# Kernel tuning notes

Measured on AMD Instinct MI355X. Metric: run time of the kernel, lower is better.

The kernel has to match this reference:

```python
import jax, jax.numpy as jnp
import numpy as np

N_BITS = 6
N_ENTRIES = 1 << N_BITS  # 64 LUT entries per node
B, IN, OUT = 1024, 1024, 2048


def setup_inputs() -> dict:
    key = jax.random.key(0)
    k1, k2, k3 = jax.random.split(key, 3)
    x = jax.random.uniform(k1, (B, IN), dtype=jnp.float32)          # soft bits in [0,1]
    lut_table = jax.random.normal(k2, (OUT, N_ENTRIES), dtype=jnp.float32)  # per-node LUT weights
    mapping = jax.random.randint(k3, (OUT, N_BITS), 0, IN, dtype=jnp.int32)  # wires per node
    return {"x": x, "lut_table": lut_table, "mapping": mapping}


def _lut_forward(x, lut_table, mapping):
    # get_mapping: gather n input wires per output node -> [B, OUT, n]
    mapped = x[:, mapping]
    # bits[k, j] = j-th bit of entry k  -> [2^n, n]
    bits = ((jnp.arange(N_ENTRIES)[:, None] >> jnp.arange(N_BITS)[None, :]) & 1
            ).astype(x.dtype)
    # Soft-AND probability of each LUT entry, built multiplicatively over the
    # n (=6) fan-in bits to avoid a [B,OUT,2^n,n] intermediate.
    probs = jnp.ones((x.shape[0], mapping.shape[0], N_ENTRIES), dtype=x.dtype)
    for j in range(N_BITS):
        xj = mapped[:, :, j][:, :, None]              # [B, OUT, 1]
        bj = bits[:, j][None, None, :]                # [1, 1, 2^n]
        probs = probs * (bj * xj + (1.0 - bj) * (1.0 - xj))
    # Expected LUT output per node: contract entry axis with learned table.
    return jnp.einsum('bok,ok->bo', probs, lut_table)


def reference(x, lut_table, mapping):
    return _lut_forward(x, lut_table, mapping)
```

## Files before the change

### kernel.cpp

```cpp
#include <hip/hip_runtime.h>

#define B_DIM   1024
#define IN_DIM  1024
#define OUT_DIM 2048
#define NBITS   6
#define NENT    64

__global__ __launch_bounds__(256) void transpose_x(const float* __restrict__ x,
                                                   float* __restrict__ xT) {
    __shared__ float tile[32][33];
    const int bx = blockIdx.x * 32;
    const int by = blockIdx.y * 32;
    const int tx = threadIdx.x & 31;
    const int ty = threadIdx.x >> 5;
#pragma unroll
    for (int i = 0; i < 4; i++) {
        const int r = by + ty + i * 8;
        tile[ty + i * 8][tx] = x[r * IN_DIM + bx + tx];
    }
    __syncthreads();
#pragma unroll
    for (int i = 0; i < 4; i++) {
        const int r = bx + ty + i * 8;
        xT[r * B_DIM + by + tx] = tile[tx][ty + i * 8];
    }
}

__global__ __launch_bounds__(256) void lut_fwd(const float* __restrict__ xsrc,
                                               const float* __restrict__ lut,
                                               const int* __restrict__ mapping,
                                               float* __restrict__ out,
                                               int sm, int sb) {
    __shared__ float slut[NENT];
    __shared__ int   smap[NBITS];
    const int o = blockIdx.y;
    const int b = blockIdx.x * 256 + threadIdx.x;

    if (threadIdx.x < NENT)  slut[threadIdx.x] = lut[o * NENT + threadIdx.x];
    if (threadIdx.x < NBITS) smap[threadIdx.x] = mapping[o * NBITS + threadIdx.x];
    __syncthreads();

    float xv[NBITS];
#pragma unroll
    for (int j = 0; j < NBITS; j++) {
        xv[j] = xsrc[smap[j] * sm + b * sb];
    }

    float v[NENT];
#pragma unroll
    for (int k = 0; k < NENT; k++) v[k] = slut[k];

#pragma unroll
    for (int j = 0; j < NBITS; j++) {
        const float xj = xv[j];
        const float om = 1.0f - xj;
#pragma unroll
        for (int m = 0; m < (NENT >> (j + 1)); m++) {
            v[m] = fmaf(v[2 * m + 1], xj, v[2 * m] * om);
        }
    }

    out[(size_t)b * OUT_DIM + o] = v[0];
}

extern "C" void kernel_launch(void* const* d_in, const int* in_sizes, int n_in,
                              void* d_out, int out_size, void* d_ws, size_t ws_size,
                              hipStream_t stream) {
    const float* x       = (const float*)d_in[0];
    const float* lut     = (const float*)d_in[1];
    const int*   mapping = (const int*)d_in[2];
    float*       out     = (float*)d_out;

    const size_t xt_bytes = (size_t)B_DIM * IN_DIM * sizeof(float);
    const dim3 grid(B_DIM / 256, OUT_DIM);

    if (ws_size >= xt_bytes) {
        float* xT = (float*)d_ws;
        const dim3 tgrid(IN_DIM / 32, B_DIM / 32);
        transpose_x<<<tgrid, 256, 0, stream>>>(x, xT);
        lut_fwd<<<grid, 256, 0, stream>>>(xT, lut, mapping, out, B_DIM, 1);
    } else {
        lut_fwd<<<grid, 256, 0, stream>>>(x, lut, mapping, out, 1, IN_DIM);
    }
}
```

Before: 77.13 us.

## Tile batch-by-output per block and coalesce output stores via shared memory

Replaces the one-output-per-block kernel with a 64x32 batch-by-output tile, where each wave handles 8 output nodes and stages its results in shared memory. The tile is then written back so consecutive threads store consecutive output columns, replacing the strided scattered stores. LUT and mapping reads use wave-uniform addresses, so they can be served as scalar loads instead of going through shared memory and a barrier. This raises register pressure and serializes 8 nodes per thread.

```diff
diff --git a/kernel.cpp b/kernel.cpp
--- a/kernel.cpp
+++ b/kernel.cpp
@@ -5,6 +5,10 @@
 #define OUT_DIM 2048
 #define NBITS   6
 #define NENT    64
+
+#define BT      64
+#define OT      32
+#define OPT     8
 
 __global__ __launch_bounds__(256) void transpose_x(const float* __restrict__ x,
                                                    float* __restrict__ xT) {
@@ -14,52 +18,88 @@
     const int tx = threadIdx.x & 31;
     const int ty = threadIdx.x >> 5;
 #pragma unroll
-    for (int i = 0; i < 4; i++) {
-        const int r = by + ty + i * 8;
-        tile[ty + i * 8][tx] = x[r * IN_DIM + bx + tx];
+    for (int i = 0; i < 4; i++)
+        tile[ty + i * 8][tx] = x[(by + ty + i * 8) * IN_DIM + bx + tx];
+    __syncthreads();
+#pragma unroll
+    for (int i = 0; i < 4; i++)
+        xT[(bx + ty + i * 8) * B_DIM + by + tx] = tile[tx][ty + i * 8];
+}
+
+__global__ __launch_bounds__(256, 4) void lut_fwd_t(const float* __restrict__ xT,
+                                                    const float* __restrict__ lut,
+                                                    const int* __restrict__ mapping,
+                                                    float* __restrict__ out) {
+    __shared__ float tile[BT][OT + 1];
+    const int tid = threadIdx.x;
+    const int tb  = tid & (BT - 1);
+    const int tg  = __builtin_amdgcn_readfirstlane(tid >> 6);
+    const int b0  = blockIdx.x * BT;
+    const int o0  = blockIdx.y * OT;
+    const int b   = b0 + tb;
+
+#pragma unroll
+    for (int i = 0; i < OPT; i++) {
+        const int o = o0 + tg * OPT + i;
+        const float* __restrict__ lr = lut + (size_t)o * NENT;
+        const int*   __restrict__ mp = mapping + (size_t)o * NBITS;
+
+        float xv[NBITS];
+#pragma unroll
+        for (int j = 0; j < NBITS; j++)
+            xv[j] = xT[(size_t)mp[j] * B_DIM + b];
+
+        float w[NENT / 2];
+        {
+            const float xj = xv[0], om = 1.0f - xj;
+#pragma unroll
+            for (int m = 0; m < NENT / 2; m++)
+                w[m] = fmaf(lr[2 * m + 1], xj, lr[2 * m] * om);
+        }
+#pragma unroll
+        for (int j = 1; j < NBITS; j++) {
+            const float xj = xv[j], om = 1.0f - xj;
+#pragma unroll
+            for (int m = 0; m < (NENT >> (j + 1)); m++)
+                w[m] = fmaf(w[2 * m + 1], xj, w[2 * m] * om);
+        }
+        tile[tb][tg * OPT + i] = w[0];
     }
     __syncthreads();
+
 #pragma unroll
-    for (int i = 0; i < 4; i++) {
-        const int r = bx + ty + i * 8;
-        xT[r * B_DIM + by + tx] = tile[tx][ty + i * 8];
+    for (int s = 0; s < (BT * OT) / 256; s++) {
+        const int f  = s * 256 + tid;
+        const int bb = f >> 5;
+        const int cc = f & (OT - 1);
+        out[(size_t)(b0 + bb) * OUT_DIM + o0 + cc] = tile[bb][cc];
     }
 }
 
-__global__ __launch_bounds__(256) void lut_fwd(const float* __restrict__ xsrc,
-                                               const float* __restrict__ lut,
-                                               const int* __restrict__ mapping,
-                                               float* __restrict__ out,
-                                               int sm, int sb) {
+__global__ __launch_bounds__(256) void lut_fwd_fallback(const float* __restrict__ x,
+                                                        const float* __restrict__ lut,
+                                                        const int* __restrict__ mapping,
+                                                        float* __restrict__ out) {
     __shared__ float slut[NENT];
     __shared__ int   smap[NBITS];
     const int o = blockIdx.y;
     const int b = blockIdx.x * 256 + threadIdx.x;
-
     if (threadIdx.x < NENT)  slut[threadIdx.x] = lut[o * NENT + threadIdx.x];
     if (threadIdx.x < NBITS) smap[threadIdx.x] = mapping[o * NBITS + threadIdx.x];
     __syncthreads();
-
     float xv[NBITS];
 #pragma unroll
-    for (int j = 0; j < NBITS; j++) {
-        xv[j] = xsrc[smap[j] * sm + b * sb];
-    }
-
+    for (int j = 0; j < NBITS; j++) xv[j] = x[(size_t)b * IN_DIM + smap[j]];
     float v[NENT];
 #pragma unroll
     for (int k = 0; k < NENT; k++) v[k] = slut[k];
-
 #pragma unroll
     for (int j = 0; j < NBITS; j++) {
-        const float xj = xv[j];
-        const float om = 1.0f - xj;
+        const float xj = xv[j], om = 1.0f - xj;
 #pragma unroll
-        for (int m = 0; m < (NENT >> (j + 1)); m++) {
+        for (int m = 0; m < (NENT >> (j + 1)); m++)
             v[m] = fmaf(v[2 * m + 1], xj, v[2 * m] * om);
-        }
     }
-
     out[(size_t)b * OUT_DIM + o] = v[0];
 }
 
@@ -72,14 +112,15 @@
     float*       out     = (float*)d_out;
 
     const size_t xt_bytes = (size_t)B_DIM * IN_DIM * sizeof(float);
-    const dim3 grid(B_DIM / 256, OUT_DIM);
 
     if (ws_size >= xt_bytes) {
         float* xT = (float*)d_ws;
         const dim3 tgrid(IN_DIM / 32, B_DIM / 32);
         transpose_x<<<tgrid, 256, 0, stream>>>(x, xT);
-        lut_fwd<<<grid, 256, 0, stream>>>(xT, lut, mapping, out, B_DIM, 1);
+        const dim3 grid(B_DIM / BT, OUT_DIM / OT);
+        lut_fwd_t<<<grid, 256, 0, stream>>>(xT, lut, mapping, out);
     } else {
-        lut_fwd<<<grid, 256, 0, stream>>>(x, lut, mapping, out, 1, IN_DIM);
+        const dim3 grid(B_DIM / 256, OUT_DIM);
+        lut_fwd_fallback<<<grid, 256, 0, stream>>>(x, lut, mapping, out);
     }
 }
```

Result: no change. 76.98 us (-0.2%).

## Fuse transpose into LUT kernel with Möbius-transformed tables and smem-staged x rows

Applied to the files above, without the earlier changes.

Drops the separate transpose kernel. Each thread now owns one output node and keeps that node's 64-entry table in registers, after converting it once with a Möbius (inclusion-exclusion) transform so each sample needs only a chain of fmas with no (1-x) terms. A block stages 16 rows of x in shared memory and gathers each node's six inputs from there, so output writes are coalesced along the node axis. The cost is heavy register use (64 coefficients plus 32 temporaries) and a 64KB+ shared tile that limits occupancy. The transformed-coefficient form may also differ slightly from the reference in rounding.

```diff
diff --git a/kernel.cpp b/kernel.cpp
--- a/kernel.cpp
+++ b/kernel.cpp
@@ -6,61 +6,85 @@
 #define NBITS   6
 #define NENT    64
 
-__global__ __launch_bounds__(256) void transpose_x(const float* __restrict__ x,
-                                                   float* __restrict__ xT) {
-    __shared__ float tile[32][33];
-    const int bx = blockIdx.x * 32;
-    const int by = blockIdx.y * 32;
-    const int tx = threadIdx.x & 31;
-    const int ty = threadIdx.x >> 5;
+#define OB   256
+#define BB   16
+#define LROW 65
+
+__global__ __launch_bounds__(256, 2) void lut_fused(
+    const float* __restrict__ x,
+    const float* __restrict__ lut,
+    const int*   __restrict__ mapping,
+    float*       __restrict__ out)
+{
+    __shared__ __align__(16) float smem[OB * LROW];
+    const int tid = threadIdx.x;
+    const int o0  = blockIdx.x * OB;
+    const int b0  = blockIdx.y * BB;
+    const int o   = o0 + tid;
+
+    const float4* lsrc = (const float4*)(lut + (size_t)o0 * NENT);
 #pragma unroll
-    for (int i = 0; i < 4; i++) {
-        const int r = by + ty + i * 8;
-        tile[ty + i * 8][tx] = x[r * IN_DIM + bx + tx];
+    for (int i = 0; i < (OB * NENT / 4) / 256; i++) {
+        const int f   = i * 256 + tid;
+        const float4 val = lsrc[f];
+        const int ow  = f >> 4;
+        const int kw  = (f & 15) * 4;
+        float* d = &smem[ow * LROW + kw];
+        d[0] = val.x; d[1] = val.y; d[2] = val.z; d[3] = val.w;
     }
+
+    int mp[NBITS];
+#pragma unroll
+    for (int j = 0; j < NBITS; j++) mp[j] = mapping[(size_t)o * NBITS + j];
+
     __syncthreads();
-#pragma unroll
-    for (int i = 0; i < 4; i++) {
-        const int r = bx + ty + i * 8;
-        xT[r * B_DIM + by + tx] = tile[tx][ty + i * 8];
-    }
-}
-
-__global__ __launch_bounds__(256) void lut_fwd(const float* __restrict__ xsrc,
-                                               const float* __restrict__ lut,
-                                               const int* __restrict__ mapping,
-                                               float* __restrict__ out,
-                                               int sm, int sb) {
-    __shared__ float slut[NENT];
-    __shared__ int   smap[NBITS];
-    const int o = blockIdx.y;
-    const int b = blockIdx.x * 256 + threadIdx.x;
-
-    if (threadIdx.x < NENT)  slut[threadIdx.x] = lut[o * NENT + threadIdx.x];
-    if (threadIdx.x < NBITS) smap[threadIdx.x] = mapping[o * NBITS + threadIdx.x];
-    __syncthreads();
-
-    float xv[NBITS];
-#pragma unroll
-    for (int j = 0; j < NBITS; j++) {
-        xv[j] = xsrc[smap[j] * sm + b * sb];
-    }
 
     float v[NENT];
 #pragma unroll
-    for (int k = 0; k < NENT; k++) v[k] = slut[k];
+    for (int k = 0; k < NENT; k++) v[k] = smem[tid * LROW + k];
 
 #pragma unroll
     for (int j = 0; j < NBITS; j++) {
-        const float xj = xv[j];
-        const float om = 1.0f - xj;
 #pragma unroll
-        for (int m = 0; m < (NENT >> (j + 1)); m++) {
-            v[m] = fmaf(v[2 * m + 1], xj, v[2 * m] * om);
+        for (int k = 0; k < NENT; k++) {
+            if ((k >> j) & 1) v[k] -= v[k ^ (1 << j)];
         }
     }
 
-    out[(size_t)b * OUT_DIM + o] = v[0];
+    __syncthreads();
+
+    const float4* xsrc = (const float4*)(x + (size_t)b0 * IN_DIM);
+    float4* xdst = (float4*)smem;
+#pragma unroll
+    for (int i = 0; i < (BB * IN_DIM / 4) / 256; i++) {
+        const int f = i * 256 + tid;
+        xdst[f] = xsrc[f];
+    }
+    __syncthreads();
+
+#pragma unroll 4
+    for (int bi = 0; bi < BB; bi++) {
+        const float* xr = &smem[bi * IN_DIM];
+        float xv[NBITS];
+#pragma unroll
+        for (int j = 0; j < NBITS; j++) xv[j] = xr[mp[j]];
+
+        float w[NENT / 2];
+        {
+            const float xj = xv[0];
+#pragma unroll
+            for (int m = 0; m < NENT / 2; m++)
+                w[m] = fmaf(xj, v[2 * m + 1], v[2 * m]);
+        }
+#pragma unroll
+        for (int j = 1; j < NBITS; j++) {
+            const float xj = xv[j];
+#pragma unroll
+            for (int m = 0; m < (NENT >> (j + 1)); m++)
+                w[m] = fmaf(xj, w[2 * m + 1], w[2 * m]);
+        }
+        out[(size_t)(b0 + bi) * OUT_DIM + o] = w[0];
+    }
 }
 
 extern "C" void kernel_launch(void* const* d_in, const int* in_sizes, int n_in,
@@ -70,16 +94,8 @@
     const float* lut     = (const float*)d_in[1];
     const int*   mapping = (const int*)d_in[2];
     float*       out     = (float*)d_out;
+    (void)d_ws; (void)ws_size;
 
-    const size_t xt_bytes = (size_t)B_DIM * IN_DIM * sizeof(float);
-    const dim3 grid(B_DIM / 256, OUT_DIM);
-
-    if (ws_size >= xt_bytes) {
-        float* xT = (float*)d_ws;
-        const dim3 tgrid(IN_DIM / 32, B_DIM / 32);
-        transpose_x<<<tgrid, 256, 0, stream>>>(x, xT);
-        lut_fwd<<<grid, 256, 0, stream>>>(xT, lut, mapping, out, B_DIM, 1);
-    } else {
-        lut_fwd<<<grid, 256, 0, stream>>>(x, lut, mapping, out, 1, IN_DIM);
-    }
+    const dim3 grid(OUT_DIM / OB, B_DIM / BB);
+    lut_fused<<<grid, 256, 0, stream>>>(x, lut, mapping, out);
 }
```

After: 69.45 us (median of 2 runs). 1.11x faster.
